# Kernel tuning notes

Measured on AMD Instinct MI355X. Metric: run time of the kernel, lower is better.

Reference implementation:

```python
import jax, jax.numpy as jnp
import numpy as np

N_NODES = 50000
N_EDGES = 800000
N_GRAPHS = 64
F_IN, F_HID, F_OUT = 128, 128, 16


def _graph_conv(x, W, b, src, dst, activation=None):
    """DGL GraphConv with norm='both': D_out^{-1/2} A^T D_in^{-1/2} X W + b."""
    n = x.shape[0]
    ones = jnp.ones((src.shape[0],), dtype=x.dtype)
    deg_out = jnp.clip(jax.ops.segment_sum(ones, src, num_segments=n), 1.0)
    deg_in = jnp.clip(jax.ops.segment_sum(ones, dst, num_segments=n), 1.0)
    h = x * jax.lax.rsqrt(deg_out)[:, None]          # scale by src out-degree
    agg = jax.ops.segment_sum(h[src], dst, num_segments=n)  # gather+scatter-add
    agg = agg * jax.lax.rsqrt(deg_in)[:, None]       # scale by dst in-degree
    out = agg @ W + b
    if activation is not None:
        out = activation(out)
    return out


def setup_inputs() -> dict:
    key = jax.random.key(0)
    ks = jax.random.split(key, 6)
    x = jax.random.normal(ks[0], (N_NODES, F_IN), dtype=jnp.float32)
    W1 = jax.random.normal(ks[1], (F_IN, F_HID), dtype=jnp.float32) * (F_IN ** -0.5)
    b1 = jnp.zeros((F_HID,), dtype=jnp.float32)
    W2 = jax.random.normal(ks[2], (F_HID, F_OUT), dtype=jnp.float32) * (F_HID ** -0.5)
    b2 = jnp.zeros((F_OUT,), dtype=jnp.float32)
    src = jax.random.randint(ks[3], (N_EDGES,), 0, N_NODES, dtype=jnp.int32)
    dst = jax.random.randint(ks[4], (N_EDGES,), 0, N_NODES, dtype=jnp.int32)
    graph_ids = jnp.sort(jax.random.randint(ks[5], (N_NODES,), 0, N_GRAPHS, dtype=jnp.int32))
    return {"x": x, "W1": W1, "b1": b1, "W2": W2, "b2": b2,
            "src": src, "dst": dst, "graph_ids": graph_ids}


def reference(x, W1, b1, W2, b2, src, dst, graph_ids):
    h = _graph_conv(x, W1, b1, src, dst, activation=jax.nn.relu)
    h = _graph_conv(h, W2, b2, src, dst, activation=None)
    # dgl.mean_nodes: per-graph mean over nodes
    sums = jax.ops.segment_sum(h, graph_ids, num_segments=N_GRAPHS)
    counts = jnp.clip(jax.ops.segment_sum(jnp.ones((N_NODES,), h.dtype), graph_ids,
                                          num_segments=N_GRAPHS), 1.0)
    return sums / counts[:, None]
```

## Files before the change

### kernel.cpp

```cpp
#include <hip/hip_runtime.h>
#include <hip/hip_bf16.h>

#define N_NODES_C 50000
#define N_EDGES_C 800000
#define N_GRAPHS_C 64
#define NBKT 782
#define BKTP 784
#define CHUNK 4096
#define NBLK_E 196

typedef __attribute__((ext_vector_type(8))) short bf16x8;
typedef __attribute__((ext_vector_type(4))) float f32x4;

__device__ __forceinline__ unsigned short f2bf(float f) {
    unsigned u = __float_as_uint(f);
    unsigned r = (u + 0x7FFFu + ((u >> 16) & 1u)) >> 16;
    return (unsigned short)r;
}

__global__ __launch_bounds__(256) void k_hist(
    const int* __restrict__ src, const int* __restrict__ dst,
    int* __restrict__ hmatD, int* __restrict__ hmatS, int nE)
{
    __shared__ int hD[BKTP], hS[BKTP];
    const int tid = threadIdx.x, blk = blockIdx.x;
    for (int i = tid; i < BKTP; i += 256) { hD[i] = 0; hS[i] = 0; }
    __syncthreads();
    const int base = blk * CHUNK;
    for (int i = tid; i < CHUNK; i += 256) {
        int e = base + i;
        if (e < nE) {
            atomicAdd(&hD[dst[e] >> 6], 1);
            atomicAdd(&hS[src[e] >> 6], 1);
        }
    }
    __syncthreads();
    for (int i = tid; i < BKTP; i += 256) {
        hmatD[blk * BKTP + i] = hD[i];
        hmatS[blk * BKTP + i] = hS[i];
    }
}

__global__ __launch_bounds__(1024) void k_bscan(
    const int* __restrict__ hmatD, const int* __restrict__ hmatS,
    int* __restrict__ bbaseD, int* __restrict__ bbaseS,
    float* __restrict__ accbuf)
{
    __shared__ int part[1024];
    const int tid = threadIdx.x;
    const int* hm = blockIdx.x ? hmatS : hmatD;
    int* bb = blockIdx.x ? bbaseS : bbaseD;
    if (blockIdx.x == 0) accbuf[tid] = 0.f;
    int v = 0;
    if (tid < NBKT)
        for (int blk = 0; blk < NBLK_E; ++blk) v += hm[blk * BKTP + tid];
    part[tid] = v;
    __syncthreads();
    for (int off = 1; off < 1024; off <<= 1) {
        int t = (tid >= off) ? part[tid - off] : 0;
        __syncthreads();
        part[tid] += t;
        __syncthreads();
    }
    if (tid < NBKT) bb[tid] = part[tid] - v;
    if (tid == NBKT - 1) bb[NBKT] = part[tid];
}

__global__ __launch_bounds__(256) void k_boff(
    const int* __restrict__ hmatD, const int* __restrict__ hmatS,
    const int* __restrict__ bbaseD, const int* __restrict__ bbaseS,
    int* __restrict__ offmatD, int* __restrict__ offmatS,
    const float* __restrict__ W1, const float* __restrict__ W2,
    unsigned short* __restrict__ w1f, unsigned short* __restrict__ w2f)
{
    __shared__ int part[256];
    const int b = blockIdx.x, tid = threadIdx.x;
    const int* hm = blockIdx.y ? hmatS : hmatD;
    const int* bb = blockIdx.y ? bbaseS : bbaseD;
    int* om = blockIdx.y ? offmatS : offmatD;
    int v = (tid < NBLK_E) ? hm[tid * BKTP + b] : 0;
    part[tid] = v;
    __syncthreads();
    for (int off = 1; off < 256; off <<= 1) {
        int t = (tid >= off) ? part[tid - off] : 0;
        __syncthreads();
        part[tid] += t;
        __syncthreads();
    }
    if (tid < NBLK_E) om[tid * BKTP + b] = bb[b] + part[tid] - v;

    if (blockIdx.y == 1 && b < 9) {
        int t = b * 256 + tid;
        if (t < 2048) {
            int kk = t >> 9, nt = (t >> 6) & 7, l = t & 63;
            int kb = kk * 32 + ((l >> 4) << 3), n = nt * 16 + (l & 15);
            ushort4 lo, hi;
            lo.x = f2bf(W1[(kb + 0) * 128 + n]); lo.y = f2bf(W1[(kb + 1) * 128 + n]);
            lo.z = f2bf(W1[(kb + 2) * 128 + n]); lo.w = f2bf(W1[(kb + 3) * 128 + n]);
            hi.x = f2bf(W1[(kb + 4) * 128 + n]); hi.y = f2bf(W1[(kb + 5) * 128 + n]);
            hi.z = f2bf(W1[(kb + 6) * 128 + n]); hi.w = f2bf(W1[(kb + 7) * 128 + n]);
            ((ushort4*)(w1f + t * 8))[0] = lo;
            ((ushort4*)(w1f + t * 8))[1] = hi;
        } else if (t < 2304) {
            int t2 = t - 2048;
            int kk = t2 >> 6, l = t2 & 63;
            int kb = kk * 32 + ((l >> 4) << 3), n = l & 15;
            ushort4 lo, hi;
            lo.x = f2bf(W2[(kb + 0) * 16 + n]); lo.y = f2bf(W2[(kb + 1) * 16 + n]);
            lo.z = f2bf(W2[(kb + 2) * 16 + n]); lo.w = f2bf(W2[(kb + 3) * 16 + n]);
            hi.x = f2bf(W2[(kb + 4) * 16 + n]); hi.y = f2bf(W2[(kb + 5) * 16 + n]);
            hi.z = f2bf(W2[(kb + 6) * 16 + n]); hi.w = f2bf(W2[(kb + 7) * 16 + n]);
            ((ushort4*)(w2f + t2 * 8))[0] = lo;
            ((ushort4*)(w2f + t2 * 8))[1] = hi;
        }
    }
}

__global__ __launch_bounds__(256) void k_scat(
    const int* __restrict__ src, const int* __restrict__ dst,
    const int* __restrict__ offmatD, const int* __restrict__ offmatS,
    unsigned* __restrict__ ed, unsigned char* __restrict__ es, int nE)
{
    __shared__ int curD[BKTP], curS[BKTP];
    const int tid = threadIdx.x, blk = blockIdx.x;
    for (int i = tid; i < BKTP; i += 256) {
        curD[i] = offmatD[blk * BKTP + i];
        curS[i] = offmatS[blk * BKTP + i];
    }
    __syncthreads();
    const int base = blk * CHUNK;
    for (int i = tid; i < CHUNK; i += 256) {
        int e = base + i;
        if (e < nE) {
            unsigned s = (unsigned)src[e], d = (unsigned)dst[e];
            int pD = atomicAdd(&curD[d >> 6], 1);
            ed[pD] = (d << 16) | s;
            int pS = atomicAdd(&curS[s >> 6], 1);
            es[pS] = (unsigned char)(s & 63u);
        }
    }
}

__global__ __launch_bounds__(256) void k_bucket(
    const unsigned* __restrict__ ed, const unsigned char* __restrict__ es,
    const int* __restrict__ bbaseD, const int* __restrict__ bbaseS,
    const float* __restrict__ x,
    int* __restrict__ rowptr, float* __restrict__ rsI, float* __restrict__ rsO,
    unsigned short* __restrict__ csr_src, unsigned short* __restrict__ xs, int nV)
{
    __shared__ int cnt[64], cur[64];
    __shared__ float rs[64];
    const int tid = threadIdx.x;
    const int side = (blockIdx.x >= NBKT);
    const int b = side ? blockIdx.x - NBKT : blockIdx.x;

    if (tid < 64) cnt[tid] = 0;
    __syncthreads();

    if (!side) {
        const int lo = bbaseD[b], hi = bbaseD[b + 1];
        for (int j = lo + tid; j < hi; j += 256)
            atomicAdd(&cnt[(ed[j] >> 16) & 63u], 1);
        __syncthreads();
        if (tid < 64) {
            int c = cnt[tid];
            int v = c;
#pragma unroll
            for (int off = 1; off < 64; off <<= 1) {
                int n = __shfl_up(v, off, 64);
                if (tid >= off) v += n;
            }
            int excl = v - c;
            int node = b * 64 + tid;
            if (node <= nV) rowptr[node] = lo + excl;
            if (node < nV) rsI[node] = rsqrtf((float)max(c, 1));
            cur[tid] = excl;
        }
        __syncthreads();
        for (int j = lo + tid; j < hi; j += 256) {
            unsigned v = ed[j];
            int p = atomicAdd(&cur[(v >> 16) & 63u], 1);
            csr_src[lo + p] = (unsigned short)(v & 0xFFFFu);
        }
    } else {
        const int lo = bbaseS[b], hi = bbaseS[b + 1];
        for (int j = lo + tid; j < hi; j += 256)
            atomicAdd(&cnt[es[j]], 1);
        __syncthreads();
        if (tid < 64) {
            int node = b * 64 + tid;
            float r = rsqrtf((float)max(cnt[tid], 1));
            if (node < nV) rsO[node] = r;
            rs[tid] = r;
        }
        __syncthreads();
        for (int q = tid; q < 64 * 32; q += 256) {
            int n = q >> 5, c = q & 31;
            int node = b * 64 + n;
            if (node < nV) {
                float wgt = rs[n];
                float4 a = ((const float4*)(x + (size_t)node * 128))[c];
                ushort4 o;
                o.x = f2bf(a.x * wgt); o.y = f2bf(a.y * wgt);
                o.z = f2bf(a.z * wgt); o.w = f2bf(a.w * wgt);
                ((ushort4*)(xs + (size_t)node * 128))[c] = o;
            }
        }
    }
}

#define ACC8(vv)                                         \
    acc[0] += __uint_as_float((vv).x << 16);             \
    acc[1] += __uint_as_float((vv).x & 0xFFFF0000u);     \
    acc[2] += __uint_as_float((vv).y << 16);             \
    acc[3] += __uint_as_float((vv).y & 0xFFFF0000u);     \
    acc[4] += __uint_as_float((vv).z << 16);             \
    acc[5] += __uint_as_float((vv).z & 0xFFFF0000u);     \
    acc[6] += __uint_as_float((vv).w << 16);             \
    acc[7] += __uint_as_float((vv).w & 0xFFFF0000u);

__global__ __launch_bounds__(256) void k_fused(
    const unsigned short* __restrict__ xs, const int* __restrict__ rowptr,
    const unsigned short* __restrict__ csr_src, const float* __restrict__ rsI,
    const float* __restrict__ b1, const unsigned short* __restrict__ w1f,
    const unsigned short* __restrict__ w2f, const float* __restrict__ rsO,
    unsigned short* __restrict__ y, int nV)
{
    __shared__ __align__(16) unsigned short Al[64 * 136];
    const int tid = threadIdx.x;
    const int w = tid >> 6, l = tid & 63;
    const int g = l >> 4, fl = l & 15;
    const int row0 = blockIdx.x * 64;

    for (int n = 0; n < 16; ++n) {
        int r = w * 16 + n;
        int v = row0 + r;
        float acc[8];
#pragma unroll
        for (int k = 0; k < 8; ++k) acc[k] = 0.f;
        float ri = 0.f;
        if (v < nV) {
            ri = rsI[v];
            int beg = rowptr[v], end = rowptr[v + 1];
            int j = beg + g;
            while (j + 12 < end) {
                int s0 = csr_src[j], s1 = csr_src[j + 4], s2 = csr_src[j + 8], s3 = csr_src[j + 12];
                uint4 w0 = *(const uint4*)(xs + (size_t)s0 * 128 + fl * 8);
                uint4 w1 = *(const uint4*)(xs + (size_t)s1 * 128 + fl * 8);
                uint4 w2 = *(const uint4*)(xs + (size_t)s2 * 128 + fl * 8);
                uint4 w3 = *(const uint4*)(xs + (size_t)s3 * 128 + fl * 8);
                ACC8(w0); ACC8(w1); ACC8(w2); ACC8(w3);
                j += 16;
            }
            while (j + 4 < end) {
                int s0 = csr_src[j], s1 = csr_src[j + 4];
                uint4 w0 = *(const uint4*)(xs + (size_t)s0 * 128 + fl * 8);
                uint4 w1 = *(const uint4*)(xs + (size_t)s1 * 128 + fl * 8);
                ACC8(w0); ACC8(w1);
                j += 8;
            }
            if (j < end) {
                int s0 = csr_src[j];
                uint4 w0 = *(const uint4*)(xs + (size_t)s0 * 128 + fl * 8);
                ACC8(w0);
            }
        }
#pragma unroll
        for (int k = 0; k < 8; ++k) {
            acc[k] += __shfl_xor(acc[k], 16, 64);
            acc[k] += __shfl_xor(acc[k], 32, 64);
        }
        if (g < 2) {
            ushort4 o;
            o.x = f2bf(acc[g * 4 + 0] * ri);
            o.y = f2bf(acc[g * 4 + 1] * ri);
            o.z = f2bf(acc[g * 4 + 2] * ri);
            o.w = f2bf(acc[g * 4 + 3] * ri);
            *(ushort4*)(&Al[r * 136 + fl * 8 + g * 4]) = o;
        }
    }

    const int lr = fl, lg = g;
    bf16x8 a[4];
#pragma unroll
    for (int kk = 0; kk < 4; ++kk)
        a[kk] = *(const bf16x8*)(&Al[(w * 16 + lr) * 136 + kk * 32 + lg * 8]);

    f32x4 acc1[8];
#pragma unroll
    for (int nt = 0; nt < 8; ++nt) acc1[nt] = (f32x4){0.f, 0.f, 0.f, 0.f};
#pragma unroll
    for (int nt = 0; nt < 8; ++nt)
#pragma unroll
        for (int kk = 0; kk < 4; ++kk) {
            bf16x8 b = *(const bf16x8*)(w1f + ((kk * 8 + nt) * 64 + l) * 8);
            acc1[nt] = __builtin_amdgcn_mfma_f32_16x16x32_bf16(a[kk], b, acc1[nt], 0, 0, 0);
        }

#pragma unroll
    for (int nt = 0; nt < 8; ++nt) {
        float bb = b1[nt * 16 + lr];
#pragma unroll
        for (int i = 0; i < 4; ++i) {
            float h = fmaxf(acc1[nt][i] + bb, 0.f);
            Al[(w * 16 + lg * 4 + i) * 136 + nt * 16 + lr] = f2bf(h);
        }
    }

    f32x4 acc2 = (f32x4){0.f, 0.f, 0.f, 0.f};
#pragma unroll
    for (int kk = 0; kk < 4; ++kk) {
        bf16x8 a2 = *(const bf16x8*)(&Al[(w * 16 + lr) * 136 + kk * 32 + lg * 8]);
        bf16x8 b2 = *(const bf16x8*)(w2f + (kk * 64 + l) * 8);
        acc2 = __builtin_amdgcn_mfma_f32_16x16x32_bf16(a2, b2, acc2, 0, 0, 0);
    }
#pragma unroll
    for (int i = 0; i < 4; ++i) {
        int r = row0 + w * 16 + lg * 4 + i;
        if (r < nV) y[(size_t)r * 16 + lr] = f2bf(acc2[i] * rsO[r]);
    }
}

__global__ __launch_bounds__(256) void k_agg2p(
    const unsigned short* __restrict__ y, const int* __restrict__ rowptr,
    const unsigned short* __restrict__ csr_src, const float* __restrict__ rsI,
    const int* __restrict__ gid, float* __restrict__ accbuf, int nV)
{
    const int tid = threadIdx.x;
    const int lane = tid & 63, f = lane & 15, g4 = lane >> 4;
    const int wid = blockIdx.x * 4 + (tid >> 6);
    int v0 = wid * 8;
    if (v0 >= nV) return;
    int vend = min(v0 + 8, nV);
    float racc = 0.f;
    int curg = gid[v0];
    for (int v = v0; v < vend; ++v) {
        int beg = rowptr[v], end = rowptr[v + 1];
        float acc = 0.f;
        int j = beg + g4;
        while (j + 4 < end) {
            int s0 = csr_src[j], s1 = csr_src[j + 4];
            unsigned u0 = y[(size_t)s0 * 16 + f];
            unsigned u1 = y[(size_t)s1 * 16 + f];
            acc += __uint_as_float(u0 << 16) + __uint_as_float(u1 << 16);
            j += 8;
        }
        if (j < end) {
            unsigned u = y[(size_t)csr_src[j] * 16 + f];
            acc += __uint_as_float(u << 16);
        }
        acc += __shfl_xor(acc, 16, 64);
        acc += __shfl_xor(acc, 32, 64);
        int gg = gid[v];
        if (gg != curg) {
            if (g4 == 0 && racc != 0.f) unsafeAtomicAdd(&accbuf[curg * 16 + f], racc);
            racc = 0.f;
            curg = gg;
        }
        racc += acc * rsI[v];
    }
    if (g4 == 0 && racc != 0.f) unsafeAtomicAdd(&accbuf[curg * 16 + f], racc);
}

__device__ __forceinline__ int lowerb(const int* __restrict__ a, int n, int key) {
    int lo = 0, hi = n;
    while (lo < hi) { int m = (lo + hi) >> 1; if (a[m] < key) lo = m + 1; else hi = m; }
    return lo;
}

__global__ __launch_bounds__(256) void k_fin(
    const float* __restrict__ accbuf, const int* __restrict__ gid,
    const float* __restrict__ b2, float* __restrict__ out, int nV)
{
    int t = threadIdx.x;
    int g = t >> 2, f0 = (t & 3) * 4;
    int lo = lowerb(gid, nV, g);
    int hi = lowerb(gid, nV, g + 1);
    int n = hi - lo;
    float inv = (n > 0) ? 1.f / (float)n : 0.f;
#pragma unroll
    for (int k = 0; k < 4; ++k) {
        int f = f0 + k;
        out[g * 16 + f] = (n > 0) ? accbuf[g * 16 + f] * inv + b2[f] : 0.f;
    }
}

extern "C" void kernel_launch(void* const* d_in, const int* in_sizes, int n_in,
                              void* d_out, int out_size, void* d_ws, size_t ws_size,
                              hipStream_t stream) {
    const float* x   = (const float*)d_in[0];
    const float* W1  = (const float*)d_in[1];
    const float* b1  = (const float*)d_in[2];
    const float* W2  = (const float*)d_in[3];
    const float* b2  = (const float*)d_in[4];
    const int*   src = (const int*)d_in[5];
    const int*   dst = (const int*)d_in[6];
    const int*   gid = (const int*)d_in[7];
    float* out = (float*)d_out;

    int* p = (int*)d_ws;
    int*   bbaseD  = p;            p += 800;
    int*   bbaseS  = p;            p += 800;
    int*   rowptr  = p;            p += 50432;
    float* rsO     = (float*)p;    p += 50176;
    float* rsI     = (float*)p;    p += 50176;
    unsigned short* csr_src = (unsigned short*)p; p += 400128;
    unsigned short* w1f = (unsigned short*)p;     p += 8192;
    unsigned short* w2f = (unsigned short*)p;     p += 1024;
    unsigned short* y   = (unsigned short*)p;     p += 401408;
    float* accbuf  = (float*)p;    p += 1024;
    unsigned short* xs = (unsigned short*)p;      p += 3211264;
    int*   hmatD   = p;            p += 153664;
    int*   hmatS   = p;            p += 153664;
    int*   offmatD = p;            p += 153664;
    int*   offmatS = p;            p += 153664;
    unsigned*      ed = (unsigned*)p;      p += 800000;
    unsigned char* es = (unsigned char*)p; p += 200000;

    k_hist <<<NBLK_E, 256, 0, stream>>>(src, dst, hmatD, hmatS, N_EDGES_C);
    k_bscan<<<2, 1024, 0, stream>>>(hmatD, hmatS, bbaseD, bbaseS, accbuf);
    k_boff <<<dim3(NBKT, 2), 256, 0, stream>>>(hmatD, hmatS, bbaseD, bbaseS,
                                               offmatD, offmatS, W1, W2, w1f, w2f);
    k_scat <<<NBLK_E, 256, 0, stream>>>(src, dst, offmatD, offmatS, ed, es, N_EDGES_C);
    k_bucket<<<2 * NBKT, 256, 0, stream>>>(ed, es, bbaseD, bbaseS, x,
                                           rowptr, rsI, rsO, csr_src, xs, N_NODES_C);

    k_fused<<<NBKT, 256, 0, stream>>>(xs, rowptr, csr_src, rsI, b1, w1f, w2f, rsO, y, N_NODES_C);
    k_agg2p<<<(N_NODES_C + 31) / 32, 256, 0, stream>>>(y, rowptr, csr_src, rsI, gid, accbuf, N_NODES_C);
    k_fin  <<<1, 256, 0, stream>>>(accbuf, gid, b2, out, N_NODES_C);
}
```

Baseline: 133.3 us.

## Split fused aggregation+MFMA kernel into a one-wave-per-node gather and a separate GEMM

Replaces the fused kernel, where each wave walked 16 nodes one after another before running the MFMA layers, with two kernels. The first assigns one wave per node for the neighbour gather and writes the bf16 aggregate to a new global buffer. The second loads that buffer and runs both dense layers with MFMA. The aim is more waves in flight to hide gather latency, at the cost of an extra kernel launch and a round trip of the aggregate through global memory.

```diff
diff --git a/kernel.cpp b/kernel.cpp
--- a/kernel.cpp
+++ b/kernel.cpp
@@ -219,82 +219,86 @@
     acc[6] += __uint_as_float((vv).w << 16);             \
     acc[7] += __uint_as_float((vv).w & 0xFFFF0000u);
 
-__global__ __launch_bounds__(256) void k_fused(
+__global__ __launch_bounds__(256) void k_agg1b(
     const unsigned short* __restrict__ xs, const int* __restrict__ rowptr,
     const unsigned short* __restrict__ csr_src, const float* __restrict__ rsI,
-    const float* __restrict__ b1, const unsigned short* __restrict__ w1f,
-    const unsigned short* __restrict__ w2f, const float* __restrict__ rsO,
-    unsigned short* __restrict__ y, int nV)
-{
-    __shared__ __align__(16) unsigned short Al[64 * 136];
+    unsigned short* __restrict__ agg1b, int nV)
+{
+    long long t = (long long)blockIdx.x * blockDim.x + threadIdx.x;
+    int v = (int)(t >> 6);
+    int lane = (int)(t & 63);
+    if (v >= nV) return;
+    int g = lane >> 4, fl = lane & 15;
+    int beg = rowptr[v], end = rowptr[v + 1];
+    float acc[8];
+#pragma unroll
+    for (int k = 0; k < 8; ++k) acc[k] = 0.f;
+
+    int j = beg + g;
+    while (j + 12 < end) {
+        int s0 = csr_src[j], s1 = csr_src[j + 4], s2 = csr_src[j + 8], s3 = csr_src[j + 12];
+        uint4 w0 = *(const uint4*)(xs + (size_t)s0 * 128 + fl * 8);
+        uint4 w1 = *(const uint4*)(xs + (size_t)s1 * 128 + fl * 8);
+        uint4 w2 = *(const uint4*)(xs + (size_t)s2 * 128 + fl * 8);
+        uint4 w3 = *(const uint4*)(xs + (size_t)s3 * 128 + fl * 8);
+        ACC8(w0); ACC8(w1); ACC8(w2); ACC8(w3);
+        j += 16;
+    }
+    while (j + 4 < end) {
+        int s0 = csr_src[j], s1 = csr_src[j + 4];
+        uint4 w0 = *(const uint4*)(xs + (size_t)s0 * 128 + fl * 8);
+        uint4 w1 = *(const uint4*)(xs + (size_t)s1 * 128 + fl * 8);
+        ACC8(w0); ACC8(w1);
+        j += 8;
+    }
+    if (j < end) {
+        int s = csr_src[j];
+        uint4 w0 = *(const uint4*)(xs + (size_t)s * 128 + fl * 8);
+        ACC8(w0);
+    }
+#pragma unroll
+    for (int k = 0; k < 8; ++k) {
+        acc[k] += __shfl_xor(acc[k], 16, 64);
+        acc[k] += __shfl_xor(acc[k], 32, 64);
+    }
+    float ri = rsI[v];
+    if (g < 2) {
+        ushort4 o;
+        o.x = f2bf(acc[g * 4 + 0] * ri);
+        o.y = f2bf(acc[g * 4 + 1] * ri);
+        o.z = f2bf(acc[g * 4 + 2] * ri);
+        o.w = f2bf(acc[g * 4 + 3] * ri);
+        *(ushort4*)(agg1b + (size_t)v * 128 + fl * 8 + g * 4) = o;
+    }
+}
+
+__global__ __launch_bounds__(256) void k_mfma(
+    const unsigned short* __restrict__ agg1b, const float* __restrict__ b1,
+    const unsigned short* __restrict__ w1f, const unsigned short* __restrict__ w2f,
+    const float* __restrict__ rsO, unsigned short* __restrict__ y, int nV)
+{
+    __shared__ __align__(16) unsigned short h1[64 * 136];
     const int tid = threadIdx.x;
     const int w = tid >> 6, l = tid & 63;
-    const int g = l >> 4, fl = l & 15;
+    const int lr = l & 15, lg = l >> 4;
     const int row0 = blockIdx.x * 64;
 
-    for (int n = 0; n < 16; ++n) {
-        int r = w * 16 + n;
-        int v = row0 + r;
-        float acc[8];
-#pragma unroll
-        for (int k = 0; k < 8; ++k) acc[k] = 0.f;
-        float ri = 0.f;
-        if (v < nV) {
-            ri = rsI[v];
-            int beg = rowptr[v], end = rowptr[v + 1];
-            int j = beg + g;
-            while (j + 12 < end) {
-                int s0 = csr_src[j], s1 = csr_src[j + 4], s2 = csr_src[j + 8], s3 = csr_src[j + 12];
-                uint4 w0 = *(const uint4*)(xs + (size_t)s0 * 128 + fl * 8);
-                uint4 w1 = *(const uint4*)(xs + (size_t)s1 * 128 + fl * 8);
-                uint4 w2 = *(const uint4*)(xs + (size_t)s2 * 128 + fl * 8);
-                uint4 w3 = *(const uint4*)(xs + (size_t)s3 * 128 + fl * 8);
-                ACC8(w0); ACC8(w1); ACC8(w2); ACC8(w3);
-                j += 16;
-            }
-            while (j + 4 < end) {
-                int s0 = csr_src[j], s1 = csr_src[j + 4];
-                uint4 w0 = *(const uint4*)(xs + (size_t)s0 * 128 + fl * 8);
-                uint4 w1 = *(const uint4*)(xs + (size_t)s1 * 128 + fl * 8);
-                ACC8(w0); ACC8(w1);
-                j += 8;
-            }
-            if (j < end) {
-                int s0 = csr_src[j];
-                uint4 w0 = *(const uint4*)(xs + (size_t)s0 * 128 + fl * 8);
-                ACC8(w0);
-            }
-        }
-#pragma unroll
-        for (int k = 0; k < 8; ++k) {
-            acc[k] += __shfl_xor(acc[k], 16, 64);
-            acc[k] += __shfl_xor(acc[k], 32, 64);
-        }
-        if (g < 2) {
-            ushort4 o;
-            o.x = f2bf(acc[g * 4 + 0] * ri);
-            o.y = f2bf(acc[g * 4 + 1] * ri);
-            o.z = f2bf(acc[g * 4 + 2] * ri);
-            o.w = f2bf(acc[g * 4 + 3] * ri);
-            *(ushort4*)(&Al[r * 136 + fl * 8 + g * 4]) = o;
-        }
-    }
-
-    const int lr = fl, lg = g;
     bf16x8 a[4];
+    const unsigned short* abase = agg1b + (size_t)(row0 + w * 16 + lr) * 128 + lg * 8;
 #pragma unroll
     for (int kk = 0; kk < 4; ++kk)
-        a[kk] = *(const bf16x8*)(&Al[(w * 16 + lr) * 136 + kk * 32 + lg * 8]);
-
-    f32x4 acc1[8];
-#pragma unroll
-    for (int nt = 0; nt < 8; ++nt) acc1[nt] = (f32x4){0.f, 0.f, 0.f, 0.f};
+        a[kk] = *(const bf16x8*)(abase + kk * 32);
+
+    f32x4 acc[8];
+#pragma unroll
+    for (int nt = 0; nt < 8; ++nt) acc[nt] = (f32x4){0.f, 0.f, 0.f, 0.f};
+
 #pragma unroll
     for (int nt = 0; nt < 8; ++nt)
 #pragma unroll
         for (int kk = 0; kk < 4; ++kk) {
             bf16x8 b = *(const bf16x8*)(w1f + ((kk * 8 + nt) * 64 + l) * 8);
-            acc1[nt] = __builtin_amdgcn_mfma_f32_16x16x32_bf16(a[kk], b, acc1[nt], 0, 0, 0);
+            acc[nt] = __builtin_amdgcn_mfma_f32_16x16x32_bf16(a[kk], b, acc[nt], 0, 0, 0);
         }
 
 #pragma unroll
@@ -302,15 +306,16 @@
         float bb = b1[nt * 16 + lr];
 #pragma unroll
         for (int i = 0; i < 4; ++i) {
-            float h = fmaxf(acc1[nt][i] + bb, 0.f);
-            Al[(w * 16 + lg * 4 + i) * 136 + nt * 16 + lr] = f2bf(h);
-        }
-    }
+            float h = fmaxf(acc[nt][i] + bb, 0.f);
+            h1[(w * 16 + lg * 4 + i) * 136 + nt * 16 + lr] = f2bf(h);
+        }
+    }
+    __syncthreads();
 
     f32x4 acc2 = (f32x4){0.f, 0.f, 0.f, 0.f};
 #pragma unroll
     for (int kk = 0; kk < 4; ++kk) {
-        bf16x8 a2 = *(const bf16x8*)(&Al[(w * 16 + lr) * 136 + kk * 32 + lg * 8]);
+        bf16x8 a2 = *(const bf16x8*)(&h1[(w * 16 + lr) * 136 + kk * 32 + lg * 8]);
         bf16x8 b2 = *(const bf16x8*)(w2f + (kk * 64 + l) * 8);
         acc2 = __builtin_amdgcn_mfma_f32_16x16x32_bf16(a2, b2, acc2, 0, 0, 0);
     }
@@ -409,7 +414,8 @@
     unsigned short* w2f = (unsigned short*)p;     p += 1024;
     unsigned short* y   = (unsigned short*)p;     p += 401408;
     float* accbuf  = (float*)p;    p += 1024;
-    unsigned short* xs = (unsigned short*)p;      p += 3211264;
+    unsigned short* xs    = (unsigned short*)p;   p += 3211264;
+    unsigned short* agg1b = (unsigned short*)p;   p += 3211264;
     int*   hmatD   = p;            p += 153664;
     int*   hmatS   = p;            p += 153664;
     int*   offmatD = p;            p += 153664;
@@ -425,7 +431,8 @@
     k_bucket<<<2 * NBKT, 256, 0, stream>>>(ed, es, bbaseD, bbaseS, x,
                                            rowptr, rsI, rsO, csr_src, xs, N_NODES_C);
 
-    k_fused<<<NBKT, 256, 0, stream>>>(xs, rowptr, csr_src, rsI, b1, w1f, w2f, rsO, y, N_NODES_C);
+    k_agg1b<<<(N_NODES_C * 64 + 255) / 256, 256, 0, stream>>>(xs, rowptr, csr_src, rsI, agg1b, N_NODES_C);
+    k_mfma <<<(N_NODES_C + 63) / 64, 256, 0, stream>>>(agg1b, b1, w1f, w2f, rsO, y, N_NODES_C);
     k_agg2p<<<(N_NODES_C + 31) / 32, 256, 0, stream>>>(y, rowptr, csr_src, rsI, gid, accbuf, N_NODES_C);
     k_fin  <<<1, 256, 0, stream>>>(accbuf, gid, b2, out, N_NODES_C);
 }
```

Result: faster. 124.3 us (-6.8%).
